# Kernel optimization log

Measured on AMD Instinct MI355X. Metric: run time of the kernel, lower is better.

Reference implementation:

```python
import jax, jax.numpy as jnp
import numpy as np

TEMPERATURE = 0.07
NEG_INF = jnp.float32(-2**32 + 1)


def setup_inputs() -> dict:
    key = jax.random.key(0)
    k1, k2, k3, k4, k5 = jax.random.split(key, 5)
    N, Na, d_in, d_out, n_rel = 10000, 10000, 256, 64, 3
    x = jax.random.normal(k1, (N, d_out), dtype=jnp.float32) * 0.1
    anchor = jax.random.normal(k2, (Na, d_in), dtype=jnp.float32) * 0.1
    # xavier-uniform-like scale for wt [d_in, d_out]
    lim = float(np.sqrt(6.0 / (d_in + d_out)))
    wt = jax.random.uniform(k3, (d_in, d_out), dtype=jnp.float32, minval=-lim, maxval=lim)
    weight = jax.random.normal(k4, (n_rel,), dtype=jnp.float32)
    # sparse adjacency (materialized dense as the original does via .to_dense())
    adjs = jax.random.bernoulli(k5, 0.01, (n_rel, Na, N))
    return {"x": x, "weight": weight, "adjs": adjs, "idx": 0, "anchor": anchor, "wt": wt}


def reference(x, weight, adjs, idx, anchor, wt):
    # x: [N, d_out], anchor: [Na, d_in], wt: [d_in, d_out], adjs: [n_rel, Na, N] bool
    adj = adjs[idx]                                   # [Na, N]
    scores = (anchor @ wt) @ x.T                      # [Na, N]
    masked = jnp.where(adj, scores, NEG_INF)          # adjacency mask
    atten = jax.nn.softmax(masked / TEMPERATURE, axis=1)
    output = atten @ x                                # [Na, d_out]
    return weight[idx] * output
```

## Files before the change

### kernel.cpp

```cpp
#include <hip/hip_runtime.h>

#define NN    10000
#define NA    10000
#define DIN   256
#define DOUT  64
#define INV_T (1.0f / 0.07f)
#define CAP   1024

typedef unsigned int uv4 __attribute__((ext_vector_type(4)));


__global__ __launch_bounds__(256) void attn_kernel(
    const float* __restrict__ x,
    const float* __restrict__ weight,
    const unsigned int* __restrict__ adjs,
    const int*   __restrict__ idxp,
    const float* __restrict__ anchor,
    const float* __restrict__ wt,
    float* __restrict__ out)
{
    __shared__ float arow[DIN];
    __shared__ float pr[DOUT];
    __shared__ int   jl[CAP];
    __shared__ float ps[CAP];
    __shared__ float red[256];
    __shared__ float wred[8];
    __shared__ int   cnt;

    const int t    = threadIdx.x;
    const int row  = blockIdx.x;
    const int w    = t >> 6;
    const int lane = t & 63;

    if (t < 64) ((float4*)arow)[t] =
        ((const float4*)(anchor + (size_t)row * DIN))[t];
    if (t == 0) cnt = 0;
    __syncthreads();

    const int idx = idxp[0];

    {
        const uv4* ar = (const uv4*)(adjs + ((size_t)idx * NA + row) * NN);
#pragma unroll
        for (int it = 0; it < 10; ++it) {
            const int cch = t + 256 * it;
            if (cch < NN / 4) {
                uv4 v = __builtin_nontemporal_load(ar + cch);
                if (v.x | v.y | v.z | v.w) {
                    unsigned int ws4[4] = {v.x, v.y, v.z, v.w};
#pragma unroll
                    for (int ww = 0; ww < 4; ++ww) {
                        if (ws4[ww]) {
                            int pos = atomicAdd(&cnt, 1);
                            if (pos < CAP) jl[pos] = cch * 4 + ww;
                        }
                    }
                }
            }
        }
    }

    {
        const int seg = t >> 6, c = t & 63;
        float acc = 0.f;
        const int k0 = seg * 64;
#pragma unroll 8
        for (int k = k0; k < k0 + 64; ++k)
            acc = fmaf(arow[k], wt[k * DOUT + c], acc);
        red[t] = acc;
    }
    __syncthreads();

    if (t < DOUT) pr[t] = red[t] + red[64 + t] + red[128 + t] + red[192 + t];
    int nc = cnt; if (nc > CAP) nc = CAP;
    __syncthreads();

    if (nc == 0) {
        if (t < DOUT) out[(size_t)row * DOUT + t] = 0.f;
        return;
    }

    {
        const int g = t >> 4, l = t & 15;
        const float4 pv = ((const float4*)pr)[l];
        for (int s = g; s < nc; s += 16) {
            const int j = jl[s];
            float4 xv = ((const float4*)(x + (size_t)j * DOUT))[l];
            float d = xv.x * pv.x + xv.y * pv.y + xv.z * pv.z + xv.w * pv.w;
            d += __shfl_xor(d, 1);
            d += __shfl_xor(d, 2);
            d += __shfl_xor(d, 4);
            d += __shfl_xor(d, 8);
            if (l == 0) ps[s] = d * INV_T;
        }
    }
    __syncthreads();

    float lm = -3.4e38f;
    for (int s = t; s < nc; s += 256) lm = fmaxf(lm, ps[s]);
#pragma unroll
    for (int o = 32; o > 0; o >>= 1) lm = fmaxf(lm, __shfl_xor(lm, o));
    if (lane == 0) wred[w] = lm;
    __syncthreads();
    const float m = fmaxf(fmaxf(wred[0], wred[1]), fmaxf(wred[2], wred[3]));

    float lsum = 0.f;
    for (int s = t; s < nc; s += 256) {
        float p = __expf(ps[s] - m);
        ps[s] = p;
        lsum += p;
    }
#pragma unroll
    for (int o = 32; o > 0; o >>= 1) lsum += __shfl_xor(lsum, o);
    if (lane == 0) wred[4 + w] = lsum;
    __syncthreads();
    const float scale = weight[idx] /
        (wred[4] + wred[5] + wred[6] + wred[7]);

    {
        const int c = t & 63, seg = t >> 6;
        float acc = 0.f;
        for (int s = seg; s < nc; s += 4)
            acc = fmaf(ps[s], x[(size_t)jl[s] * DOUT + c], acc);
        red[t] = acc;
        __syncthreads();
        if (t < DOUT) {
            float o = (red[t] + red[64 + t] + red[128 + t] + red[192 + t]) * scale;
            __builtin_nontemporal_store(o, out + (size_t)row * DOUT + t);
        }
    }
}

extern "C" void kernel_launch(void* const* d_in, const int* in_sizes, int n_in,
                              void* d_out, int out_size, void* d_ws, size_t ws_size,
                              hipStream_t stream) {
    const float*        x      = (const float*)d_in[0];
    const float*        weight = (const float*)d_in[1];
    const unsigned int* adjs   = (const unsigned int*)d_in[2];
    const int*          idxp   = (const int*)d_in[3];
    const float*        anchor = (const float*)d_in[4];
    const float*        wt     = (const float*)d_in[5];
    float*              out    = (float*)d_out;

    attn_kernel<<<NA, 256, 0, stream>>>(x, weight, adjs, idxp, anchor, wt, out);
}
```

Measured before the change: 1.418 ms.

## Fuse score, softmax and weighted sum into single-pass online softmax per wave

Replaces the three-phase score/max/exp-sum/accumulate pipeline with an online-softmax loop in which each wave owns whole neighbor rows, computes each dot product via a full-wave shuffle reduction, and accumulates the exp-weighted x row on the fly. This avoids reading each gathered x row twice and removes the ps scratch array and two block barriers. In exchange it performs 64-lane shuffle reductions per neighbor and extra exp calls for rescaling. The kernel is likely dominated by streaming the 400MB adjacency row mask, so the gain may be small.

```diff
diff --git a/kernel.cpp b/kernel.cpp
--- a/kernel.cpp
+++ b/kernel.cpp
@@ -22,7 +22,6 @@
     __shared__ float arow[DIN];
     __shared__ float pr[DOUT];
     __shared__ int   jl[CAP];
-    __shared__ float ps[CAP];
     __shared__ float red[256];
     __shared__ float wred[8];
     __shared__ int   cnt;
@@ -80,54 +79,54 @@
         return;
     }
 
-    {
-        const int g = t >> 4, l = t & 15;
-        const float4 pv = ((const float4*)pr)[l];
-        for (int s = g; s < nc; s += 16) {
-            const int j = jl[s];
-            float4 xv = ((const float4*)(x + (size_t)j * DOUT))[l];
-            float d = xv.x * pv.x + xv.y * pv.y + xv.z * pv.z + xv.w * pv.w;
-            d += __shfl_xor(d, 1);
-            d += __shfl_xor(d, 2);
-            d += __shfl_xor(d, 4);
-            d += __shfl_xor(d, 8);
-            if (l == 0) ps[s] = d * INV_T;
+    const float prc = pr[lane];
+    float m_w = -3.4e38f, l_w = 0.f, acc = 0.f;
+    int s = w;
+    for (; s + 4 < nc; s += 8) {
+        const int j0 = jl[s], j1 = jl[s + 4];
+        const float xv0 = x[(size_t)j0 * DOUT + lane];
+        const float xv1 = x[(size_t)j1 * DOUT + lane];
+        float d0 = prc * xv0, d1 = prc * xv1;
+#pragma unroll
+        for (int o = 32; o > 0; o >>= 1) {
+            d0 += __shfl_xor(d0, o);
+            d1 += __shfl_xor(d1, o);
         }
+        d0 *= INV_T; d1 *= INV_T;
+        const float mnew  = fmaxf(m_w, fmaxf(d0, d1));
+        const float alpha = __expf(m_w - mnew);
+        const float p0    = __expf(d0 - mnew);
+        const float p1    = __expf(d1 - mnew);
+        acc = acc * alpha + p0 * xv0 + p1 * xv1;
+        l_w = l_w * alpha + p0 + p1;
+        m_w = mnew;
     }
-    __syncthreads();
+    if (s < nc) {
+        const int j = jl[s];
+        const float xv = x[(size_t)j * DOUT + lane];
+        float d = prc * xv;
+#pragma unroll
+        for (int o = 32; o > 0; o >>= 1) d += __shfl_xor(d, o);
+        d *= INV_T;
+        const float mnew  = fmaxf(m_w, d);
+        const float alpha = __expf(m_w - mnew);
+        const float p     = __expf(d - mnew);
+        acc = acc * alpha + p * xv;
+        l_w = l_w * alpha + p;
+        m_w = mnew;
+    }
 
-    float lm = -3.4e38f;
-    for (int s = t; s < nc; s += 256) lm = fmaxf(lm, ps[s]);
-#pragma unroll
-    for (int o = 32; o > 0; o >>= 1) lm = fmaxf(lm, __shfl_xor(lm, o));
-    if (lane == 0) wred[w] = lm;
+    if (lane == 0) wred[w] = m_w;
     __syncthreads();
     const float m = fmaxf(fmaxf(wred[0], wred[1]), fmaxf(wred[2], wred[3]));
-
-    float lsum = 0.f;
-    for (int s = t; s < nc; s += 256) {
-        float p = __expf(ps[s] - m);
-        ps[s] = p;
-        lsum += p;
-    }
-#pragma unroll
-    for (int o = 32; o > 0; o >>= 1) lsum += __shfl_xor(lsum, o);
-    if (lane == 0) wred[4 + w] = lsum;
+    const float f = __expf(m_w - m);
+    if (lane == 0) wred[4 + w] = l_w * f;
+    red[t] = acc * f;
     __syncthreads();
-    const float scale = weight[idx] /
-        (wred[4] + wred[5] + wred[6] + wred[7]);
-
-    {
-        const int c = t & 63, seg = t >> 6;
-        float acc = 0.f;
-        for (int s = seg; s < nc; s += 4)
-            acc = fmaf(ps[s], x[(size_t)jl[s] * DOUT + c], acc);
-        red[t] = acc;
-        __syncthreads();
-        if (t < DOUT) {
-            float o = (red[t] + red[64 + t] + red[128 + t] + red[192 + t]) * scale;
-            __builtin_nontemporal_store(o, out + (size_t)row * DOUT + t);
-        }
+    const float scale = weight[idx] / (wred[4] + wred[5] + wred[6] + wred[7]);
+    if (t < DOUT) {
+        float o = (red[t] + red[64 + t] + red[128 + t] + red[192 + t]) * scale;
+        __builtin_nontemporal_store(o, out + (size_t)row * DOUT + t);
     }
 }
 
```

Result: no change. 1.401 ms (-1.2%).
